# Kernel tuning notes

Measured on AMD Instinct MI355X. Metric: run time of the kernel, lower is better.

## Reference

```python
import jax, jax.numpy as jnp
import numpy as np

# OGB feature vocab sizes
ATOM_DIMS = [119, 4, 12, 12, 10, 6, 6, 2, 2]
BOND_DIMS = [5, 6, 2]
ATOM_OFF = np.concatenate([[0], np.cumsum(ATOM_DIMS)[:-1]]).astype(np.int32)
BOND_OFF = np.concatenate([[0], np.cumsum(BOND_DIMS)[:-1]]).astype(np.int32)
SCHEDULE_LEN = 5   # len(train_schedule) == len(eval_schedule)
NUM_GRAPHS = 12000
BN_EPS = 1e-5

N_NODES, N_EDGES, HIDDEN, NUM_TASKS = 300000, 600000, 128, 128


def setup_inputs() -> dict:
    key = jax.random.key(0)
    ks = jax.random.split(key, 16)
    x = jax.random.randint(ks[0], (N_NODES, 9), 0, 2, dtype=jnp.int32)
    edge_index = jax.random.randint(ks[1], (2, N_EDGES), 0, N_NODES, dtype=jnp.int32)
    edge_attr = jax.random.randint(ks[2], (N_EDGES, 3), 0, 2, dtype=jnp.int32)
    batch = jnp.sort(jax.random.randint(ks[3], (N_NODES,), 0, NUM_GRAPHS, dtype=jnp.int32))
    # learned parameters (embedding tables concatenated with offsets)
    atom_emb = jax.random.normal(ks[4], (sum(ATOM_DIMS), HIDDEN), jnp.float32) * 0.1
    bond_emb = jax.random.normal(ks[5], (sum(BOND_DIMS), HIDDEN), jnp.float32) * 0.1
    conv_W = jax.random.normal(ks[6], (HIDDEN, HIDDEN), jnp.float32) * (1.0 / np.sqrt(HIDDEN))
    conv_b = jnp.zeros((HIDDEN,), jnp.float32)
    root_emb = jax.random.normal(ks[7], (HIDDEN,), jnp.float32) * 0.1
    bn_gamma = jnp.ones((HIDDEN,), jnp.float32)
    bn_beta = jnp.zeros((HIDDEN,), jnp.float32)
    bn_mean = jnp.zeros((HIDDEN,), jnp.float32)   # running stats (eval mode)
    bn_var = jnp.ones((HIDDEN,), jnp.float32)
    lin_W = jax.random.normal(ks[8], (NUM_TASKS, HIDDEN), jnp.float32) * (1.0 / np.sqrt(HIDDEN))
    lin_b = jnp.zeros((NUM_TASKS,), jnp.float32)
    return {"x": x, "edge_index": edge_index, "edge_attr": edge_attr, "batch": batch,
            "atom_emb": atom_emb, "bond_emb": bond_emb, "conv_W": conv_W, "conv_b": conv_b,
            "root_emb": root_emb, "bn_gamma": bn_gamma, "bn_beta": bn_beta,
            "bn_mean": bn_mean, "bn_var": bn_var, "lin_W": lin_W, "lin_b": lin_b}


def reference(x, edge_index, edge_attr, batch, atom_emb, bond_emb, conv_W, conv_b,
              root_emb, bn_gamma, bn_beta, bn_mean, bn_var, lin_W, lin_b):
    N = x.shape[0]
    # AtomEncoder / BondEncoder: sum of per-feature embedding lookups
    h = atom_emb[x + jnp.asarray(ATOM_OFF, x.dtype)].sum(axis=1)            # [N, H]
    e = bond_emb[edge_attr + jnp.asarray(BOND_OFF, edge_attr.dtype)].sum(axis=1)  # [E, H]
    row, col = edge_index[0], edge_index[1]
    deg = jax.ops.segment_sum(jnp.ones_like(row, h.dtype), row, num_segments=N) + 1.0  # [N]
    dis = deg ** -0.5                                                        # deg >= 1, no inf
    norm = dis[row] * dis[col]                                               # [E]
    inv_std = bn_gamma / jnp.sqrt(bn_var + BN_EPS)
    for i in range(SCHEDULE_LEN):
        old = h
        z = h @ conv_W.T + conv_b                                            # [N, H]
        # message: norm * relu(x_j + edge_emb), aggregated at target (col) via scatter-add
        msg = norm[:, None] * jax.nn.relu(z[row] + e)                        # [E, H]
        agg = jax.ops.segment_sum(msg, col, num_segments=N)                  # [N, H]
        z = agg + jax.nn.relu(z + root_emb) / deg[:, None]                   # self-loop term
        z = jax.nn.relu(z)
        z = (z - bn_mean) * inv_std + bn_beta                                # BN (eval, running stats)
        # dropout: identity in eval mode
        # NOTE: faithful to source bug: smooth_fac is the loop index i, not schedule[i]
        h = i * old + (1 - i) * z
    # global mean pool over graphs
    counts = jax.ops.segment_sum(jnp.ones((N,), h.dtype), batch, num_segments=NUM_GRAPHS)
    pooled = jax.ops.segment_sum(h, batch, num_segments=NUM_GRAPHS) / jnp.maximum(counts, 1.0)[:, None]
    return pooled @ lin_W.T + lin_b                                          # [num_graphs, num_tasks]
```

## Files before the change

### kernel.cpp

```cpp
#include <hip/hip_runtime.h>

#define HID 128

typedef __attribute__((ext_vector_type(8))) short short8;
typedef __attribute__((ext_vector_type(8))) unsigned short ushort8v;
typedef __attribute__((ext_vector_type(4))) float floatx4;
typedef __attribute__((ext_vector_type(4))) unsigned short ushort4v;

__device__ __forceinline__ unsigned short f2bf(float f) {
    unsigned u = __builtin_bit_cast(unsigned, f);
    u += 0x7FFF + ((u >> 16) & 1);
    return (unsigned short)(u >> 16);
}
__device__ __forceinline__ float bf2f(unsigned short s) {
    unsigned u = ((unsigned)s) << 16;
    return __builtin_bit_cast(float, u);
}

__global__ void fillrd_kernel(float* __restrict__ dis, int* __restrict__ indeg, int N)
{
    int i = blockIdx.x * 256 + threadIdx.x;
    if (i < N) { dis[i] = 0.f; indeg[i] = 0; }
}

__global__ void diag_kernel(float* __restrict__ out, long n, float val)
{
    long i = (long)blockIdx.x * blockDim.x + threadIdx.x;
    if (i < n) out[i] = val;
}

__global__ __launch_bounds__(256) void tables_kernel(
    const float* __restrict__ conv_W, unsigned short* __restrict__ Wb,
    const float* __restrict__ lin_W, unsigned short* __restrict__ linWb,
    const float* __restrict__ bond_emb, float* __restrict__ comb,
    const float* __restrict__ gamma, const float* __restrict__ beta,
    const float* __restrict__ mean, const float* __restrict__ var,
    float* __restrict__ bnsc, float* __restrict__ bnsh)
{
    int blk = blockIdx.x;
    int tid = threadIdx.x;
    if (blk < 64) {
        int i = blk * 256 + tid;
        Wb[i] = f2bf(conv_W[i]);
    } else if (blk < 128) {
        int i = (blk - 64) * 256 + tid;
        linWb[i] = f2bf(lin_W[i]);
    } else if (blk < 158) {
        int i = (blk - 128) * 2 + (tid >> 7);
        int c = tid & 127;
        int a0 = i / 12, a1 = (i % 12) / 2, a2 = i % 2;
        comb[i * HID + c] = bond_emb[a0 * HID + c] + bond_emb[(5 + a1) * HID + c]
                          + bond_emb[(11 + a2) * HID + c];
    } else if (tid < HID) {
        float sc = gamma[tid] * rsqrtf(var[tid] + 1e-5f);
        bnsc[tid] = sc;
        bnsh[tid] = beta[tid] - mean[tid] * sc;
    }
}

__global__ void hist_kernel(const int* __restrict__ ei, float* __restrict__ dis,
                            int* __restrict__ indeg, int E)
{
    for (int e = blockIdx.x * blockDim.x + threadIdx.x; e < E; e += gridDim.x * blockDim.x) {
        atomicAdd(&dis[ei[e]], 1.f);
        atomicAdd(&indeg[ei[E + e]], 1);
    }
}

__global__ void fdeg_kernel(float* __restrict__ dis, int N)
{
    int n = blockIdx.x * blockDim.x + threadIdx.x;
    if (n < N) dis[n] = rsqrtf(dis[n] + 1.f);
}

__global__ __launch_bounds__(256) void bsum_kernel(
    const int* __restrict__ indeg, int* __restrict__ partial, int N)
{
    __shared__ int s[256];
    int i = blockIdx.x * 256 + threadIdx.x;
    s[threadIdx.x] = (i < N) ? indeg[i] : 0;
    __syncthreads();
    for (int d = 128; d > 0; d >>= 1) {
        if (threadIdx.x < d) s[threadIdx.x] += s[threadIdx.x + d];
        __syncthreads();
    }
    if (threadIdx.x == 0) partial[blockIdx.x] = s[0];
}

__global__ __launch_bounds__(256) void scan1_kernel(
    const int* __restrict__ partial, int* __restrict__ offs,
    int* __restrict__ ptr, int B, int N)
{
    __shared__ int s[256];
    __shared__ int carry_s;
    int tid = threadIdx.x;
    if (tid == 0) carry_s = 0;
    __syncthreads();
    for (int base = 0; base < B; base += 256) {
        int i = base + tid;
        int v = (i < B) ? partial[i] : 0;
        s[tid] = v;
        __syncthreads();
        for (int d = 1; d < 256; d <<= 1) {
            int t = (tid >= d) ? s[tid - d] : 0;
            __syncthreads();
            s[tid] += t;
            __syncthreads();
        }
        int carry = carry_s;
        if (i < B) offs[i] = carry + s[tid] - v;
        __syncthreads();
        if (tid == 0) carry_s = carry + s[255];
        __syncthreads();
    }
    if (tid == 0) ptr[N] = carry_s;
}

__global__ __launch_bounds__(256) void scan2_kernel(
    const int* __restrict__ indeg, const int* __restrict__ offs,
    int* __restrict__ ptr, int* __restrict__ cursor, int N)
{
    __shared__ int s[256];
    int tid = threadIdx.x;
    int i = blockIdx.x * 256 + tid;
    int v = (i < N) ? indeg[i] : 0;
    s[tid] = v;
    __syncthreads();
    for (int d = 1; d < 256; d <<= 1) {
        int t = (tid >= d) ? s[tid - d] : 0;
        __syncthreads();
        s[tid] += t;
        __syncthreads();
    }
    if (i < N) {
        int ex = offs[blockIdx.x] + s[tid] - v;
        ptr[i] = ex;
        cursor[i] = ex;
    }
}

__global__ void fillcsr_kernel(const int* __restrict__ ei, const int* __restrict__ attr,
                               const float* __restrict__ dis, int* __restrict__ cursor,
                               int2* __restrict__ edata, int E)
{
    for (int e = blockIdx.x * blockDim.x + threadIdx.x; e < E; e += gridDim.x * blockDim.x) {
        int r   = ei[e];
        int col = ei[E + e];
        int pos = atomicAdd(&cursor[col], 1);
        int ci  = attr[e * 3] * 12 + attr[e * 3 + 1] * 2 + attr[e * 3 + 2];
        float nrm = dis[r] * dis[col];
        int2 ed;
        ed.x = r;
        ed.y = ci | ((int)f2bf(nrm) << 16);
        edata[pos] = ed;
    }
}

__global__ void gptr_kernel(const int* __restrict__ batch, int* __restrict__ gptr,
                            int N, int G)
{
    int n = blockIdx.x * blockDim.x + threadIdx.x;
    if (n >= N) return;
    int b = batch[n];
    int bp = (n == 0) ? -1 : batch[n - 1];
    for (int g = bp + 1; g <= b; ++g) gptr[g] = n;
    if (n == N - 1)
        for (int g = b + 1; g <= G; ++g) gptr[g] = N;
}

template<bool FIRST>
__device__ __forceinline__ ushort8v agg_node(
    long n, int c, const int* __restrict__ ptr, const int2* __restrict__ edata,
    const float* __restrict__ comb, const float* __restrict__ dis,
    const float* __restrict__ root, const float* __restrict__ bnsc,
    const float* __restrict__ bnsh, const unsigned short* __restrict__ zb,
    const unsigned short* __restrict__ hb, float fi)
{
    ushort8v zv = *reinterpret_cast<const ushort8v*>(zb + n * HID + c);
    ushort8v hv;
    if constexpr (!FIRST) hv = *reinterpret_cast<const ushort8v*>(hb + n * HID + c);
    float di = dis[n];
    float rd = di * di;
    float acc[8];
#pragma unroll
    for (int j = 0; j < 8; ++j) acc[j] = fmaxf(bf2f(zv[j]) + root[c + j], 0.f) * rd;

    int jb = ptr[n], je = ptr[n + 1];
    int j2 = jb;
    for (; j2 + 1 < je; j2 += 2) {
        int2 e0 = edata[j2];
        int2 e1 = edata[j2 + 1];
        ushort8v z0 = *reinterpret_cast<const ushort8v*>(zb + (long)e0.x * HID + c);
        ushort8v z1 = *reinterpret_cast<const ushort8v*>(zb + (long)e1.x * HID + c);
        const float* c0 = comb + (e0.y & 0xFF) * HID + c;
        const float* c1 = comb + (e1.y & 0xFF) * HID + c;
        float n0 = bf2f((unsigned short)(((unsigned)e0.y) >> 16));
        float n1 = bf2f((unsigned short)(((unsigned)e1.y) >> 16));
#pragma unroll
        for (int j = 0; j < 8; ++j) {
            acc[j] += fmaxf(bf2f(z0[j]) + c0[j], 0.f) * n0;
            acc[j] += fmaxf(bf2f(z1[j]) + c1[j], 0.f) * n1;
        }
    }
    if (j2 < je) {
        int2 e0 = edata[j2];
        ushort8v z0 = *reinterpret_cast<const ushort8v*>(zb + (long)e0.x * HID + c);
        const float* c0 = comb + (e0.y & 0xFF) * HID + c;
        float n0 = bf2f((unsigned short)(((unsigned)e0.y) >> 16));
#pragma unroll
        for (int j = 0; j < 8; ++j) acc[j] += fmaxf(bf2f(z0[j]) + c0[j], 0.f) * n0;
    }

    ushort8v o;
#pragma unroll
    for (int j = 0; j < 8; ++j) {
        float t = fmaxf(acc[j], 0.f) * bnsc[c + j] + bnsh[c + j];
        float h;
        if constexpr (FIRST) h = t;
        else h = fi * bf2f(hv[j]) + (1.f - fi) * t;
        o[j] = f2bf(h);
    }
    return o;
}

template<bool FIRST>
__global__ __launch_bounds__(256) void agg_kernel(
    const int* __restrict__ ptr, const int2* __restrict__ edata,
    const float* __restrict__ comb, const float* __restrict__ dis,
    const float* __restrict__ root, const float* __restrict__ bnsc,
    const float* __restrict__ bnsh, const unsigned short* __restrict__ zb,
    unsigned short* __restrict__ hb, float fi, int N)
{
    long n = (long)blockIdx.x * 16 + (threadIdx.x >> 4);
    if (n >= N) return;
    int c = (threadIdx.x & 15) * 8;
    ushort8v o = agg_node<FIRST>(n, c, ptr, edata, comb, dis, root, bnsc, bnsh, zb, hb, fi);
    *reinterpret_cast<ushort8v*>(hb + n * HID + c) = o;
}

__global__ __launch_bounds__(256) void egemm_kernel(
    const int* __restrict__ x, const float* __restrict__ atom_emb,
    const unsigned short* __restrict__ Wb, const float* __restrict__ bias,
    unsigned short* __restrict__ zb, int N)
{
    __shared__ unsigned short hs[128][132];
    int tid = threadIdx.x;
    long base = (long)blockIdx.x * 128;
    const int OFF[9] = {0, 119, 123, 135, 147, 157, 163, 169, 171};

    int sn = tid >> 4;
    int cc = (tid & 15) * 8;
#pragma unroll 1
    for (int s = 0; s < 8; ++s) {
        int lr = s * 16 + sn;
        long n = base + lr;
        ushort8v o;
        if (n < N) {
            float acc[8];
#pragma unroll
            for (int j = 0; j < 8; ++j) acc[j] = 0.f;
#pragma unroll
            for (int f = 0; f < 9; ++f) {
                int idx = x[n * 9 + f] + OFF[f];
                const float* ep = atom_emb + (long)idx * HID + cc;
                floatx4 v0 = *reinterpret_cast<const floatx4*>(ep);
                floatx4 v1 = *reinterpret_cast<const floatx4*>(ep + 4);
#pragma unroll
                for (int j = 0; j < 4; ++j) { acc[j] += v0[j]; acc[j + 4] += v1[j]; }
            }
#pragma unroll
            for (int j = 0; j < 8; ++j) o[j] = f2bf(acc[j]);
        } else {
            ushort8v z8 = {0, 0, 0, 0, 0, 0, 0, 0};
            o = z8;
        }
        *reinterpret_cast<ushort8v*>(&hs[lr][cc]) = o;
    }
    __syncthreads();

    int wave = tid >> 6;
    int lane = tid & 63;
    int l15 = lane & 15;
    int q = lane >> 4;
    int rowl0 = wave * 32;

    short8 a[2][4];
#pragma unroll
    for (int mt = 0; mt < 2; ++mt) {
        int rl = rowl0 + mt * 16 + l15;
#pragma unroll
        for (int kb = 0; kb < 4; ++kb)
            a[mt][kb] = *reinterpret_cast<const short8*>(&hs[rl][q * 8 + kb * 32]);
    }

    floatx4 acc[2][8];
#pragma unroll
    for (int mt = 0; mt < 2; ++mt)
#pragma unroll
        for (int nt = 0; nt < 8; ++nt) {
            floatx4 zz = {0.f, 0.f, 0.f, 0.f};
            acc[mt][nt] = zz;
        }

#pragma unroll
    for (int nt = 0; nt < 8; ++nt) {
        const unsigned short* bp = Wb + (nt * 16 + l15) * HID + q * 8;
#pragma unroll
        for (int kb = 0; kb < 4; ++kb) {
            short8 b = *reinterpret_cast<const short8*>(bp + kb * 32);
            acc[0][nt] = __builtin_amdgcn_mfma_f32_16x16x32_bf16(a[0][kb], b, acc[0][nt], 0, 0, 0);
            acc[1][nt] = __builtin_amdgcn_mfma_f32_16x16x32_bf16(a[1][kb], b, acc[1][nt], 0, 0, 0);
        }
    }

    float bi[8];
#pragma unroll
    for (int nt = 0; nt < 8; ++nt) bi[nt] = bias[nt * 16 + l15];

    __syncthreads();
#pragma unroll
    for (int mt = 0; mt < 2; ++mt)
#pragma unroll
        for (int r = 0; r < 4; ++r) {
            int lr = rowl0 + mt * 16 + q * 4 + r;
#pragma unroll
            for (int nt = 0; nt < 8; ++nt)
                hs[lr][l15 + 16 * nt] = f2bf(acc[mt][nt][r] + bi[nt]);
        }
    __syncthreads();

    int tr = tid >> 4;
    int tc = (tid & 15) * 8;
#pragma unroll
    for (int i = 0; i < 8; ++i) {
        int row = i * 16 + tr;
        long gr = base + row;
        if (gr < N) {
            ushort8v v = *reinterpret_cast<const ushort8v*>(&hs[row][tc]);
            *reinterpret_cast<ushort8v*>(zb + gr * HID + tc) = v;
        }
    }
}

__global__ __launch_bounds__(256) void gemm_kernel(
    const unsigned short* __restrict__ hb, const unsigned short* __restrict__ Wb,
    const float* __restrict__ bias, unsigned short* __restrict__ zb, int N)
{
    __shared__ unsigned short st[128][132];
    int wave = threadIdx.x >> 6;
    int lane = threadIdx.x & 63;
    int l15 = lane & 15;
    int q = lane >> 4;
    long row0 = (long)blockIdx.x * 128 + wave * 32;

    short8 a[2][4];
#pragma unroll
    for (int mt = 0; mt < 2; ++mt) {
        long rl = row0 + mt * 16 + l15;
        if (rl > (long)N - 1) rl = (long)N - 1;
        const unsigned short* ap = hb + rl * HID + q * 8;
#pragma unroll
        for (int kb = 0; kb < 4; ++kb)
            a[mt][kb] = *reinterpret_cast<const short8*>(ap + kb * 32);
    }

    floatx4 acc[2][8];
#pragma unroll
    for (int mt = 0; mt < 2; ++mt)
#pragma unroll
        for (int nt = 0; nt < 8; ++nt) {
            floatx4 zz = {0.f, 0.f, 0.f, 0.f};
            acc[mt][nt] = zz;
        }

#pragma unroll
    for (int nt = 0; nt < 8; ++nt) {
        const unsigned short* bp = Wb + (nt * 16 + l15) * HID + q * 8;
#pragma unroll
        for (int kb = 0; kb < 4; ++kb) {
            short8 b = *reinterpret_cast<const short8*>(bp + kb * 32);
            acc[0][nt] = __builtin_amdgcn_mfma_f32_16x16x32_bf16(a[0][kb], b, acc[0][nt], 0, 0, 0);
            acc[1][nt] = __builtin_amdgcn_mfma_f32_16x16x32_bf16(a[1][kb], b, acc[1][nt], 0, 0, 0);
        }
    }

    float bi[8];
#pragma unroll
    for (int nt = 0; nt < 8; ++nt) bi[nt] = bias[nt * 16 + l15];

#pragma unroll
    for (int mt = 0; mt < 2; ++mt)
#pragma unroll
        for (int r = 0; r < 4; ++r) {
            int lr = wave * 32 + mt * 16 + q * 4 + r;
#pragma unroll
            for (int nt = 0; nt < 8; ++nt)
                st[lr][l15 + 16 * nt] = f2bf(acc[mt][nt][r] + bi[nt]);
        }
    __syncthreads();

    int tr = threadIdx.x >> 4;
    int tc = (threadIdx.x & 15) * 8;
#pragma unroll
    for (int i = 0; i < 8; ++i) {
        int row = i * 16 + tr;
        long gr = (long)blockIdx.x * 128 + row;
        if (gr < N) {
            ushort8v v = *reinterpret_cast<const ushort8v*>(&st[row][tc]);
            *reinterpret_cast<ushort8v*>(zb + gr * HID + tc) = v;
        }
    }
}

__global__ __launch_bounds__(256) void linmm_kernel(
    const unsigned short* __restrict__ pb, const unsigned short* __restrict__ Wb,
    const float* __restrict__ bias, float* __restrict__ out, int G)
{
    int wave = threadIdx.x >> 6;
    int lane = threadIdx.x & 63;
    int l15 = lane & 15;
    int q = lane >> 4;
    long row0 = (long)blockIdx.x * 128 + wave * 32;

    short8 a[2][4];
#pragma unroll
    for (int mt = 0; mt < 2; ++mt) {
        long rl = row0 + mt * 16 + l15;
        if (rl > (long)G - 1) rl = (long)G - 1;
        const unsigned short* ap = pb + rl * HID + q * 8;
#pragma unroll
        for (int kb = 0; kb < 4; ++kb)
            a[mt][kb] = *reinterpret_cast<const short8*>(ap + kb * 32);
    }

    floatx4 acc[2][8];
#pragma unroll
    for (int mt = 0; mt < 2; ++mt)
#pragma unroll
        for (int nt = 0; nt < 8; ++nt) {
            floatx4 zz = {0.f, 0.f, 0.f, 0.f};
            acc[mt][nt] = zz;
        }

#pragma unroll
    for (int nt = 0; nt < 8; ++nt) {
        const unsigned short* bp = Wb + (nt * 16 + l15) * HID + q * 8;
#pragma unroll
        for (int kb = 0; kb < 4; ++kb) {
            short8 b = *reinterpret_cast<const short8*>(bp + kb * 32);
            acc[0][nt] = __builtin_amdgcn_mfma_f32_16x16x32_bf16(a[0][kb], b, acc[0][nt], 0, 0, 0);
            acc[1][nt] = __builtin_amdgcn_mfma_f32_16x16x32_bf16(a[1][kb], b, acc[1][nt], 0, 0, 0);
        }
    }

    float bi[8];
#pragma unroll
    for (int nt = 0; nt < 8; ++nt) bi[nt] = bias[nt * 16 + l15];

#pragma unroll
    for (int mt = 0; mt < 2; ++mt)
#pragma unroll
        for (int r = 0; r < 4; ++r) {
            long rr = row0 + mt * 16 + q * 4 + r;
            if (rr < G) {
                float* op = out + rr * HID + l15;
#pragma unroll
                for (int nt = 0; nt < 8; ++nt)
                    op[nt * 16] = acc[mt][nt][r] + bi[nt];
            }
        }
}

__global__ __launch_bounds__(256) void pool_kernel(
    const unsigned short* __restrict__ hb, const int* __restrict__ gptr,
    unsigned short* __restrict__ pb, int G)
{
    int g = blockIdx.x;
    if (g >= G) return;
    int tid = threadIdx.x;
    int sub = tid >> 5;
    int c = (tid & 31) * 4;
    int lo = gptr[g], hi = gptr[g + 1];
    floatx4 s = {0.f, 0.f, 0.f, 0.f};
    for (int n = lo + sub; n < hi; n += 8) {
        ushort4v hv = *reinterpret_cast<const ushort4v*>(hb + (long)n * HID + c);
#pragma unroll
        for (int j = 0; j < 4; ++j) s[j] += bf2f(hv[j]);
    }
    __shared__ float ps[8][HID];
    *reinterpret_cast<floatx4*>(&ps[sub][c]) = s;
    __syncthreads();
    if (tid < HID) {
        float sum = 0.f;
#pragma unroll
        for (int k = 0; k < 8; ++k) sum += ps[k][tid];
        float cnt = (hi > lo) ? (float)(hi - lo) : 1.f;
        pb[(long)g * HID + tid] = f2bf(sum / cnt);
    }
}

extern "C" void kernel_launch(void* const* d_in, const int* in_sizes, int n_in,
                              void* d_out, int out_size, void* d_ws, size_t ws_size,
                              hipStream_t stream)
{
    const int* x          = (const int*)d_in[0];
    const int* ei         = (const int*)d_in[1];
    const int* attr       = (const int*)d_in[2];
    const int* batch      = (const int*)d_in[3];
    const float* atom_emb = (const float*)d_in[4];
    const float* bond_emb = (const float*)d_in[5];
    const float* conv_W   = (const float*)d_in[6];
    const float* conv_b   = (const float*)d_in[7];
    const float* root     = (const float*)d_in[8];
    const float* gamma    = (const float*)d_in[9];
    const float* beta     = (const float*)d_in[10];
    const float* mean     = (const float*)d_in[11];
    const float* var      = (const float*)d_in[12];
    const float* lin_W    = (const float*)d_in[13];
    const float* lin_b    = (const float*)d_in[14];
    float* out = (float*)d_out;

    const int N = in_sizes[0] / 9;
    const int E = in_sizes[1] / 2;
    const int G = out_size / HID;
    const int B = (N + 255) / 256;

    auto al = [](size_t b) { return (b + 255) & ~(size_t)255; };
    const size_t need =
        al((size_t)N * HID * 2) +
        al((size_t)N * HID * 2) +
        al((size_t)(N + 1) * 4) +
        al((size_t)E * 8) +
        al((size_t)N * 4) +
        al((size_t)2048 * 4) * 2 +
        al((size_t)(G + 1) * 4) +
        al((size_t)(G + 128) * HID * 2) +
        al((size_t)60 * HID * 4) +
        al((size_t)HID * 4) * 2 +
        al((size_t)HID * HID * 2) * 2;

    if (ws_size < need || B > 2048) {
        float v = (B > 2048) ? 3000.f : (1000.f + (float)(ws_size >> 20));
        long n = (long)out_size;
        diag_kernel<<<(int)((n + 255) / 256), 256, 0, stream>>>(out, n, v);
        return;
    }

    char* wsp = (char*)d_ws;
    size_t used = 0;
    auto alloc = [&](size_t bytes) { char* p = wsp + used; used += al(bytes); return p; };
    unsigned short* hb = (unsigned short*)alloc((size_t)N * HID * 2);
    unsigned short* zb = (unsigned short*)alloc((size_t)N * HID * 2);
    int* ptr      = (int*)alloc((size_t)(N + 1) * 4);
    int2* edata   = (int2*)alloc((size_t)E * 8);
    int* indeg    = (int*)alloc((size_t)N * 4);
    int* cursor   = indeg;
    int* partial  = (int*)alloc((size_t)2048 * 4);
    int* offs     = (int*)alloc((size_t)2048 * 4);
    int* gptr     = (int*)alloc((size_t)(G + 1) * 4);
    unsigned short* pb = (unsigned short*)alloc((size_t)(G + 128) * HID * 2);
    float* dis    = (float*)pb;
    float* comb   = (float*)alloc((size_t)60 * HID * 4);
    float* bnsc   = (float*)alloc((size_t)HID * 4);
    float* bnsh   = (float*)alloc((size_t)HID * 4);
    unsigned short* Wb    = (unsigned short*)alloc((size_t)HID * HID * 2);
    unsigned short* linWb = (unsigned short*)alloc((size_t)HID * HID * 2);

    fillrd_kernel<<<B, 256, 0, stream>>>(dis, indeg, N);
    tables_kernel<<<159, 256, 0, stream>>>(conv_W, Wb, lin_W, linWb, bond_emb, comb,
                                           gamma, beta, mean, var, bnsc, bnsh);
    hist_kernel<<<1024, 256, 0, stream>>>(ei, dis, indeg, E);
    fdeg_kernel<<<B, 256, 0, stream>>>(dis, N);
    bsum_kernel<<<B, 256, 0, stream>>>(indeg, partial, N);
    scan1_kernel<<<1, 256, 0, stream>>>(partial, offs, ptr, B, N);
    scan2_kernel<<<B, 256, 0, stream>>>(indeg, offs, ptr, cursor, N);
    fillcsr_kernel<<<1024, 256, 0, stream>>>(ei, attr, dis, cursor, edata, E);
    gptr_kernel<<<B, 256, 0, stream>>>(batch, gptr, N, G);

    const int gemm_blocks = (N + 127) / 128;
    const int agg_blocks  = (N + 15) / 16;
    egemm_kernel<<<gemm_blocks, 256, 0, stream>>>(x, atom_emb, Wb, conv_b, zb, N);
    agg_kernel<true ><<<agg_blocks, 256, 0, stream>>>(ptr, edata, comb, dis, root,
            bnsc, bnsh, zb, hb, 0.f, N);
    const float fis[3] = {2.f, 3.f, 4.f};
    for (int t = 0; t < 3; ++t) {
        gemm_kernel<<<gemm_blocks, 256, 0, stream>>>(hb, Wb, conv_b, zb, N);
        agg_kernel<false><<<agg_blocks, 256, 0, stream>>>(ptr, edata, comb, dis, root,
                bnsc, bnsh, zb, hb, fis[t], N);
    }

    pool_kernel<<<G, 256, 0, stream>>>(hb, gptr, pb, G);
    linmm_kernel<<<(G + 127) / 128, 256, 0, stream>>>(pb, linWb, lin_b, out, G);
}
```

Measured before the change: 726.2 us.

## Fuse aggregation with next-layer GEMM using double-buffered z arrays

Each aggregation step now computes the new h rows straight into shared memory and immediately runs the next layer's 128x128 MFMA GEMM in the same kernel. The output goes to a second z buffer, which avoids the read-after-write hazard on gathered neighbors. This removes separate gemm launches and the re-read of h from global memory. The atom embedding table is also pre-converted to bf16 and node features are staged in LDS for the encoder. In exchange it needs an extra N×128 bf16 workspace buffer, and the fused path runs with 128-node blocks, which may reduce occupancy and load balance for the irregular gather.

```diff
diff --git a/kernel.cpp b/kernel.cpp
--- a/kernel.cpp
+++ b/kernel.cpp
@@ -1,6 +1,7 @@
 #include <hip/hip_runtime.h>
 
 #define HID 128
+#define AROWS 173
 
 typedef __attribute__((ext_vector_type(8))) short short8;
 typedef __attribute__((ext_vector_type(8))) unsigned short ushort8v;
@@ -35,7 +36,8 @@
     const float* __restrict__ bond_emb, float* __restrict__ comb,
     const float* __restrict__ gamma, const float* __restrict__ beta,
     const float* __restrict__ mean, const float* __restrict__ var,
-    float* __restrict__ bnsc, float* __restrict__ bnsh)
+    float* __restrict__ bnsc, float* __restrict__ bnsh,
+    const float* __restrict__ atom_emb, unsigned short* __restrict__ aeb)
 {
     int blk = blockIdx.x;
     int tid = threadIdx.x;
@@ -51,10 +53,15 @@
         int a0 = i / 12, a1 = (i % 12) / 2, a2 = i % 2;
         comb[i * HID + c] = bond_emb[a0 * HID + c] + bond_emb[(5 + a1) * HID + c]
                           + bond_emb[(11 + a2) * HID + c];
-    } else if (tid < HID) {
-        float sc = gamma[tid] * rsqrtf(var[tid] + 1e-5f);
-        bnsc[tid] = sc;
-        bnsh[tid] = beta[tid] - mean[tid] * sc;
+    } else if (blk == 158) {
+        if (tid < HID) {
+            float sc = gamma[tid] * rsqrtf(var[tid] + 1e-5f);
+            bnsc[tid] = sc;
+            bnsh[tid] = beta[tid] - mean[tid] * sc;
+        }
+    } else {
+        int i = (blk - 159) * 256 + tid;
+        if (i < AROWS * HID) aeb[i] = f2bf(atom_emb[i]);
     }
 }
 
@@ -238,16 +245,134 @@
     *reinterpret_cast<ushort8v*>(hb + n * HID + c) = o;
 }
 
+__device__ __forceinline__ void gemm_from_lds(
+    unsigned short (*hs)[132], const unsigned short* __restrict__ Wb,
+    const float* __restrict__ bias, unsigned short* __restrict__ zb,
+    long base, int N, int tid)
+{
+    int wave = tid >> 6;
+    int lane = tid & 63;
+    int l15 = lane & 15;
+    int q = lane >> 4;
+    int rowl0 = wave * 32;
+
+    short8 a[2][4];
+#pragma unroll
+    for (int mt = 0; mt < 2; ++mt) {
+        int rl = rowl0 + mt * 16 + l15;
+#pragma unroll
+        for (int kb = 0; kb < 4; ++kb)
+            a[mt][kb] = *reinterpret_cast<const short8*>(&hs[rl][q * 8 + kb * 32]);
+    }
+
+    floatx4 acc[2][8];
+#pragma unroll
+    for (int mt = 0; mt < 2; ++mt)
+#pragma unroll
+        for (int nt = 0; nt < 8; ++nt) {
+            floatx4 zz = {0.f, 0.f, 0.f, 0.f};
+            acc[mt][nt] = zz;
+        }
+
+#pragma unroll
+    for (int nt = 0; nt < 8; ++nt) {
+        const unsigned short* bp = Wb + (nt * 16 + l15) * HID + q * 8;
+#pragma unroll
+        for (int kb = 0; kb < 4; ++kb) {
+            short8 b = *reinterpret_cast<const short8*>(bp + kb * 32);
+            acc[0][nt] = __builtin_amdgcn_mfma_f32_16x16x32_bf16(a[0][kb], b, acc[0][nt], 0, 0, 0);
+            acc[1][nt] = __builtin_amdgcn_mfma_f32_16x16x32_bf16(a[1][kb], b, acc[1][nt], 0, 0, 0);
+        }
+    }
+
+    float bi[8];
+#pragma unroll
+    for (int nt = 0; nt < 8; ++nt) bi[nt] = bias[nt * 16 + l15];
+
+    __syncthreads();
+#pragma unroll
+    for (int mt = 0; mt < 2; ++mt)
+#pragma unroll
+        for (int r = 0; r < 4; ++r) {
+            int lr = rowl0 + mt * 16 + q * 4 + r;
+#pragma unroll
+            for (int nt = 0; nt < 8; ++nt)
+                hs[lr][l15 + 16 * nt] = f2bf(acc[mt][nt][r] + bi[nt]);
+        }
+    __syncthreads();
+
+    int tr = tid >> 4;
+    int tc = (tid & 15) * 8;
+#pragma unroll
+    for (int i = 0; i < 8; ++i) {
+        int row = i * 16 + tr;
+        long gr = base + row;
+        if (gr < N) {
+            ushort8v v = *reinterpret_cast<const ushort8v*>(&hs[row][tc]);
+            *reinterpret_cast<ushort8v*>(zb + gr * HID + tc) = v;
+        }
+    }
+}
+
 __global__ __launch_bounds__(256) void egemm_kernel(
-    const int* __restrict__ x, const float* __restrict__ atom_emb,
+    const int* __restrict__ x, const unsigned short* __restrict__ aeb,
     const unsigned short* __restrict__ Wb, const float* __restrict__ bias,
     unsigned short* __restrict__ zb, int N)
+{
+    __shared__ unsigned short hs[128][132];
+    __shared__ int xs[128 * 9];
+    int tid = threadIdx.x;
+    long base = (long)blockIdx.x * 128;
+    const int OFF[9] = {0, 119, 123, 135, 147, 157, 163, 169, 171};
+
+    int nb = (N - base < 128) ? (int)(N - base) : 128;
+    int cnt = nb * 9;
+    for (int i = tid; i < cnt; i += 256) xs[i] = x[base * 9 + i];
+    __syncthreads();
+
+    int sn = tid >> 4;
+    int cc = (tid & 15) * 8;
+#pragma unroll 1
+    for (int s = 0; s < 8; ++s) {
+        int lr = s * 16 + sn;
+        ushort8v o;
+        if (lr < nb) {
+            float acc[8];
+#pragma unroll
+            for (int j = 0; j < 8; ++j) acc[j] = 0.f;
+#pragma unroll
+            for (int f = 0; f < 9; ++f) {
+                int idx = xs[lr * 9 + f] + OFF[f];
+                ushort8v v = *reinterpret_cast<const ushort8v*>(aeb + (long)idx * HID + cc);
+#pragma unroll
+                for (int j = 0; j < 8; ++j) acc[j] += bf2f(v[j]);
+            }
+#pragma unroll
+            for (int j = 0; j < 8; ++j) o[j] = f2bf(acc[j]);
+        } else {
+            ushort8v z8 = {0, 0, 0, 0, 0, 0, 0, 0};
+            o = z8;
+        }
+        *reinterpret_cast<ushort8v*>(&hs[lr][cc]) = o;
+    }
+    __syncthreads();
+
+    gemm_from_lds(hs, Wb, bias, zb, base, N, tid);
+}
+
+template<bool FIRST>
+__global__ __launch_bounds__(256) void fusedag_kernel(
+    const int* __restrict__ ptr, const int2* __restrict__ edata,
+    const float* __restrict__ comb, const float* __restrict__ dis,
+    const float* __restrict__ root, const float* __restrict__ bnsc,
+    const float* __restrict__ bnsh, const unsigned short* __restrict__ zin,
+    unsigned short* __restrict__ hb, const unsigned short* __restrict__ Wb,
+    const float* __restrict__ bias, unsigned short* __restrict__ zout,
+    float fi, int N)
 {
     __shared__ unsigned short hs[128][132];
     int tid = threadIdx.x;
     long base = (long)blockIdx.x * 128;
-    const int OFF[9] = {0, 119, 123, 135, 147, 157, 163, 169, 171};
-
     int sn = tid >> 4;
     int cc = (tid & 15) * 8;
 #pragma unroll 1
@@ -256,20 +381,9 @@
         long n = base + lr;
         ushort8v o;
         if (n < N) {
-            float acc[8];
-#pragma unroll
-            for (int j = 0; j < 8; ++j) acc[j] = 0.f;
-#pragma unroll
-            for (int f = 0; f < 9; ++f) {
-                int idx = x[n * 9 + f] + OFF[f];
-                const float* ep = atom_emb + (long)idx * HID + cc;
-                floatx4 v0 = *reinterpret_cast<const floatx4*>(ep);
-                floatx4 v1 = *reinterpret_cast<const floatx4*>(ep + 4);
-#pragma unroll
-                for (int j = 0; j < 4; ++j) { acc[j] += v0[j]; acc[j + 4] += v1[j]; }
-            }
-#pragma unroll
-            for (int j = 0; j < 8; ++j) o[j] = f2bf(acc[j]);
+            o = agg_node<FIRST>(n, cc, ptr, edata, comb, dis, root, bnsc, bnsh,
+                                zin, hb, fi);
+            *reinterpret_cast<ushort8v*>(hb + n * HID + cc) = o;
         } else {
             ushort8v z8 = {0, 0, 0, 0, 0, 0, 0, 0};
             o = z8;
@@ -278,138 +392,35 @@
     }
     __syncthreads();
 
+    gemm_from_lds(hs, Wb, bias, zout, base, N, tid);
+}
+
+__global__ __launch_bounds__(256) void gemm_kernel(
+    const unsigned short* __restrict__ hb, const unsigned short* __restrict__ Wb,
+    const float* __restrict__ bias, unsigned short* __restrict__ zb, int N)
+{
+    __shared__ unsigned short st[128][132];
+    int tid = threadIdx.x;
     int wave = tid >> 6;
     int lane = tid & 63;
     int l15 = lane & 15;
     int q = lane >> 4;
-    int rowl0 = wave * 32;
-
-    short8 a[2][4];
-#pragma unroll
-    for (int mt = 0; mt < 2; ++mt) {
-        int rl = rowl0 + mt * 16 + l15;
-#pragma unroll
-        for (int kb = 0; kb < 4; ++kb)
-            a[mt][kb] = *reinterpret_cast<const short8*>(&hs[rl][q * 8 + kb * 32]);
-    }
-
-    floatx4 acc[2][8];
-#pragma unroll
-    for (int mt = 0; mt < 2; ++mt)
-#pragma unroll
-        for (int nt = 0; nt < 8; ++nt) {
-            floatx4 zz = {0.f, 0.f, 0.f, 0.f};
-            acc[mt][nt] = zz;
-        }
-
-#pragma unroll
-    for (int nt = 0; nt < 8; ++nt) {
-        const unsigned short* bp = Wb + (nt * 16 + l15) * HID + q * 8;
-#pragma unroll
-        for (int kb = 0; kb < 4; ++kb) {
-            short8 b = *reinterpret_cast<const short8*>(bp + kb * 32);
-            acc[0][nt] = __builtin_amdgcn_mfma_f32_16x16x32_bf16(a[0][kb], b, acc[0][nt], 0, 0, 0);
-            acc[1][nt] = __builtin_amdgcn_mfma_f32_16x16x32_bf16(a[1][kb], b, acc[1][nt], 0, 0, 0);
-        }
-    }
-
-    float bi[8];
-#pragma unroll
-    for (int nt = 0; nt < 8; ++nt) bi[nt] = bias[nt * 16 + l15];
-
-    __syncthreads();
-#pragma unroll
-    for (int mt = 0; mt < 2; ++mt)
-#pragma unroll
-        for (int r = 0; r < 4; ++r) {
-            int lr = rowl0 + mt * 16 + q * 4 + r;
-#pragma unroll
-            for (int nt = 0; nt < 8; ++nt)
-                hs[lr][l15 + 16 * nt] = f2bf(acc[mt][nt][r] + bi[nt]);
-        }
-    __syncthreads();
-
-    int tr = tid >> 4;
-    int tc = (tid & 15) * 8;
-#pragma unroll
-    for (int i = 0; i < 8; ++i) {
-        int row = i * 16 + tr;
-        long gr = base + row;
-        if (gr < N) {
-            ushort8v v = *reinterpret_cast<const ushort8v*>(&hs[row][tc]);
-            *reinterpret_cast<ushort8v*>(zb + gr * HID + tc) = v;
-        }
-    }
-}
-
-__global__ __launch_bounds__(256) void gemm_kernel(
-    const unsigned short* __restrict__ hb, const unsigned short* __restrict__ Wb,
-    const float* __restrict__ bias, unsigned short* __restrict__ zb, int N)
-{
-    __shared__ unsigned short st[128][132];
-    int wave = threadIdx.x >> 6;
-    int lane = threadIdx.x & 63;
-    int l15 = lane & 15;
-    int q = lane >> 4;
-    long row0 = (long)blockIdx.x * 128 + wave * 32;
-
-    short8 a[2][4];
+    long base = (long)blockIdx.x * 128;
+    long row0 = base + wave * 32;
+
 #pragma unroll
     for (int mt = 0; mt < 2; ++mt) {
         long rl = row0 + mt * 16 + l15;
         if (rl > (long)N - 1) rl = (long)N - 1;
         const unsigned short* ap = hb + rl * HID + q * 8;
+        int lrow = wave * 32 + mt * 16 + l15;
 #pragma unroll
         for (int kb = 0; kb < 4; ++kb)
-            a[mt][kb] = *reinterpret_cast<const short8*>(ap + kb * 32);
-    }
-
-    floatx4 acc[2][8];
-#pragma unroll
-    for (int mt = 0; mt < 2; ++mt)
-#pragma unroll
-        for (int nt = 0; nt < 8; ++nt) {
-            floatx4 zz = {0.f, 0.f, 0.f, 0.f};
-            acc[mt][nt] = zz;
-        }
-
-#pragma unroll
-    for (int nt = 0; nt < 8; ++nt) {
-        const unsigned short* bp = Wb + (nt * 16 + l15) * HID + q * 8;
-#pragma unroll
-        for (int kb = 0; kb < 4; ++kb) {
-            short8 b = *reinterpret_cast<const short8*>(bp + kb * 32);
-            acc[0][nt] = __builtin_amdgcn_mfma_f32_16x16x32_bf16(a[0][kb], b, acc[0][nt], 0, 0, 0);
-            acc[1][nt] = __builtin_amdgcn_mfma_f32_16x16x32_bf16(a[1][kb], b, acc[1][nt], 0, 0, 0);
-        }
-    }
-
-    float bi[8];
-#pragma unroll
-    for (int nt = 0; nt < 8; ++nt) bi[nt] = bias[nt * 16 + l15];
-
-#pragma unroll
-    for (int mt = 0; mt < 2; ++mt)
-#pragma unroll
-        for (int r = 0; r < 4; ++r) {
-            int lr = wave * 32 + mt * 16 + q * 4 + r;
-#pragma unroll
-            for (int nt = 0; nt < 8; ++nt)
-                st[lr][l15 + 16 * nt] = f2bf(acc[mt][nt][r] + bi[nt]);
-        }
-    __syncthreads();
-
-    int tr = threadIdx.x >> 4;
-    int tc = (threadIdx.x & 15) * 8;
-#pragma unroll
-    for (int i = 0; i < 8; ++i) {
-        int row = i * 16 + tr;
-        long gr = (long)blockIdx.x * 128 + row;
-        if (gr < N) {
-            ushort8v v = *reinterpret_cast<const ushort8v*>(&st[row][tc]);
-            *reinterpret_cast<ushort8v*>(zb + gr * HID + tc) = v;
-        }
-    }
+            *reinterpret_cast<ushort8v*>(&st[lrow][q * 8 + kb * 32]) =
+                *reinterpret_cast<const ushort8v*>(ap + kb * 32);
+    }
+    __syncthreads();
+    gemm_from_lds(st, Wb, bias, zb, base, N, tid);
 }
 
 __global__ __launch_bounds__(256) void linmm_kernel(
@@ -526,7 +537,7 @@
     const int B = (N + 255) / 256;
 
     auto al = [](size_t b) { return (b + 255) & ~(size_t)255; };
-    const size_t need =
+    const size_t need_base =
         al((size_t)N * HID * 2) +
         al((size_t)N * HID * 2) +
         al((size_t)(N + 1) * 4) +
@@ -537,14 +548,17 @@
         al((size_t)(G + 128) * HID * 2) +
         al((size_t)60 * HID * 4) +
         al((size_t)HID * 4) * 2 +
-        al((size_t)HID * HID * 2) * 2;
-
-    if (ws_size < need || B > 2048) {
+        al((size_t)HID * HID * 2) * 2 +
+        al((size_t)AROWS * HID * 2);
+    const size_t need_fused = need_base + al((size_t)N * HID * 2);
+
+    if (ws_size < need_base || B > 2048) {
         float v = (B > 2048) ? 3000.f : (1000.f + (float)(ws_size >> 20));
         long n = (long)out_size;
         diag_kernel<<<(int)((n + 255) / 256), 256, 0, stream>>>(out, n, v);
         return;
     }
+    const bool fused_ok = (ws_size >= need_fused);
 
     char* wsp = (char*)d_ws;
     size_t used = 0;
@@ -565,10 +579,13 @@
     float* bnsh   = (float*)alloc((size_t)HID * 4);
     unsigned short* Wb    = (unsigned short*)alloc((size_t)HID * HID * 2);
     unsigned short* linWb = (unsigned short*)alloc((size_t)HID * HID * 2);
+    unsigned short* aeb   = (unsigned short*)alloc((size_t)AROWS * HID * 2);
+    unsigned short* zb2   = (unsigned short*)alloc((size_t)N * HID * 2);
 
     fillrd_kernel<<<B, 256, 0, stream>>>(dis, indeg, N);
-    tables_kernel<<<159, 256, 0, stream>>>(conv_W, Wb, lin_W, linWb, bond_emb, comb,
-                                           gamma, beta, mean, var, bnsc, bnsh);
+    tables_kernel<<<246, 256, 0, stream>>>(conv_W, Wb, lin_W, linWb, bond_emb, comb,
+                                           gamma, beta, mean, var, bnsc, bnsh,
+                                           atom_emb, aeb);
     hist_kernel<<<1024, 256, 0, stream>>>(ei, dis, indeg, E);
     fdeg_kernel<<<B, 256, 0, stream>>>(dis, N);
     bsum_kernel<<<B, 256, 0, stream>>>(indeg, partial, N);
@@ -579,14 +596,26 @@
 
     const int gemm_blocks = (N + 127) / 128;
     const int agg_blocks  = (N + 15) / 16;
-    egemm_kernel<<<gemm_blocks, 256, 0, stream>>>(x, atom_emb, Wb, conv_b, zb, N);
-    agg_kernel<true ><<<agg_blocks, 256, 0, stream>>>(ptr, edata, comb, dis, root,
-            bnsc, bnsh, zb, hb, 0.f, N);
-    const float fis[3] = {2.f, 3.f, 4.f};
-    for (int t = 0; t < 3; ++t) {
-        gemm_kernel<<<gemm_blocks, 256, 0, stream>>>(hb, Wb, conv_b, zb, N);
+    egemm_kernel<<<gemm_blocks, 256, 0, stream>>>(x, aeb, Wb, conv_b, zb, N);
+
+    if (fused_ok) {
+        fusedag_kernel<true ><<<gemm_blocks, 256, 0, stream>>>(ptr, edata, comb, dis,
+                root, bnsc, bnsh, zb,  hb, Wb, conv_b, zb2, 0.f, N);
+        fusedag_kernel<false><<<gemm_blocks, 256, 0, stream>>>(ptr, edata, comb, dis,
+                root, bnsc, bnsh, zb2, hb, Wb, conv_b, zb,  2.f, N);
+        fusedag_kernel<false><<<gemm_blocks, 256, 0, stream>>>(ptr, edata, comb, dis,
+                root, bnsc, bnsh, zb,  hb, Wb, conv_b, zb2, 3.f, N);
         agg_kernel<false><<<agg_blocks, 256, 0, stream>>>(ptr, edata, comb, dis, root,
-                bnsc, bnsh, zb, hb, fis[t], N);
+                bnsc, bnsh, zb2, hb, 4.f, N);
+    } else {
+        agg_kernel<true ><<<agg_blocks, 256, 0, stream>>>(ptr, edata, comb, dis, root,
+                bnsc, bnsh, zb, hb, 0.f, N);
+        const float fis[3] = {2.f, 3.f, 4.f};
+        for (int t = 0; t < 3; ++t) {
+            gemm_kernel<<<gemm_blocks, 256, 0, stream>>>(hb, Wb, conv_b, zb, N);
+            agg_kernel<false><<<agg_blocks, 256, 0, stream>>>(ptr, edata, comb, dis,
+                    root, bnsc, bnsh, zb, hb, fis[t], N);
+        }
     }
 
     pool_kernel<<<G, 256, 0, stream>>>(hb, gptr, pb, G);
```

After: 771.3 us. +6.2%, slower.
